# Performance work log

Measured on AMD Instinct MI355X. Metric: run time of the kernel, lower is better.

## Reference

```python
import jax, jax.numpy as jnp
import numpy as np
from jax import lax

DN = ('NCHW', 'OIHW', 'NCHW')
NUM_CODES = 8192


def _conv(x, w, b):
    # Conv2d(k=4, s=2, p=1)
    y = lax.conv_general_dilated(x, w, (2, 2), ((1, 1), (1, 1)), dimension_numbers=DN)
    return y + b[None, :, None, None]


def _convT(x, w, b):
    # ConvTranspose2d(k=4, s=2, p=1) as lhs-dilated conv; kernel already in equivalent OIHW layout
    y = lax.conv_general_dilated(x, w, (1, 1), ((2, 2), (2, 2)), lhs_dilation=(2, 2), dimension_numbers=DN)
    return y + b[None, :, None, None]


def _aff(x, s, b):
    # eval-mode BatchNorm folded to per-channel affine
    return x * s[None, :, None, None] + b[None, :, None, None]


def _forward(x, ew1, eb1, bn1s, bn1b, ew2, eb2, bn2s, bn2b, ew3, eb3, bn3s, bn3b, ew4, eb4, embed, cluster_size, dw1, db1, dbn1s, dbn1b, dw2, db2, dbn2s, dbn2b, dw3, db3, dbn3s, dbn3b, dw4, db4):
    sg = lax.stop_gradient
    embed = sg(embed)          # codebook is a torch buffer -> no grad
    cluster_size = sg(cluster_size)
    relu = jax.nn.relu
    # ---- Encoder: 4 stride-2 convs ----
    h = relu(_aff(_conv(x, ew1, eb1), bn1s, bn1b))
    h = relu(_aff(_conv(h, ew2, eb2), bn2s, bn2b))
    h = relu(_aff(_conv(h, ew3, eb3), bn3s, bn3b))
    z = _conv(h, ew4, eb4)                       # [B, D, G, G]
    zt = jnp.transpose(z, (0, 2, 3, 1))          # [B, G, G, D]
    D = zt.shape[-1]
    flat = zt.reshape(-1, D)                     # [N, D]
    N = flat.shape[0]
    # ---- VQ: pairwise squared distance + argmin codebook lookup ----
    dist = (flat * flat).sum(1, keepdims=True) - 2.0 * (flat @ embed.T) + (embed * embed).sum(1)[None, :]
    soft = jax.nn.softmax(-dist, axis=-1)        # temperature = 1.0
    codes = jnp.argmin(dist, axis=1)             # [N]
    zq = embed[codes]                            # [N, D]
    commitment_loss = jnp.mean((flat - sg(zq)) ** 2)
    codebook_loss = jnp.mean((zq - sg(flat)) ** 2)
    avg_soft = soft.mean(0)
    usage_entropy = -(avg_soft * jnp.log(avg_soft + 1e-10)).sum()
    diversity_loss = -usage_entropy / float(np.log(NUM_CODES))
    zq_st = flat + sg(zq - flat)                 # straight-through estimator
    zq_grid = jnp.transpose(zq_st.reshape(zt.shape), (0, 3, 1, 2))  # [B, D, G, G]
    # ---- Decoder: 4 stride-2 transposed convs ----
    h = relu(_aff(_convT(zq_grid, dw1, db1), dbn1s, dbn1b))
    h = relu(_aff(_convT(h, dw2, db2), dbn2s, dbn2b))
    h = relu(_aff(_convT(h, dw3, db3), dbn3s, dbn3b))
    recon = jax.nn.sigmoid(_convT(h, dw4, db4))
    recon_loss = jnp.mean((recon - x) ** 2)
    # ---- usage stats (no-grad in torch) ----
    hard_avg = jnp.zeros(NUM_CODES, flat.dtype).at[codes].add(1.0) / N
    perplexity = jnp.exp(-(hard_avg * jnp.log(hard_avg + 1e-10)).sum())
    active_codes = (cluster_size > 1).sum()
    codes_grid = codes.reshape(zt.shape[:-1])
    return (recon, recon_loss, codes_grid, zq_grid, commitment_loss, codebook_loss, diversity_loss, usage_entropy, perplexity, active_codes)


def setup_inputs() -> dict:
    keys = iter(jax.random.split(jax.random.key(0), 64))
    def randn(shape, s=1.0):
        return jax.random.normal(next(keys), shape, jnp.float32) * s
    def randu(shape):
        return jax.random.uniform(next(keys), shape, dtype=jnp.float32)
    B, H = 32, 256
    return {
        'x': randu((B, 1, H, H)),
        'ew1': randn((64, 1, 4, 4), 0.25), 'eb1': randn((64,), 0.1),
        'bn1s': randu((64,)), 'bn1b': randn((64,), 0.1),
        'ew2': randn((64, 64, 4, 4), 0.03), 'eb2': randn((64,), 0.1),
        'bn2s': randu((64,)), 'bn2b': randn((64,), 0.1),
        'ew3': randn((128, 64, 4, 4), 0.03), 'eb3': randn((128,), 0.1),
        'bn3s': randu((128,)), 'bn3b': randn((128,), 0.1),
        'ew4': randn((64, 128, 4, 4), 0.02), 'eb4': randn((64,), 0.1),
        'embed': randn((8192, 64), 0.5),
        'cluster_size': jnp.ones((8192,), jnp.float32),
        'dw1': randn((128, 64, 4, 4), 0.03), 'db1': randn((128,), 0.1),
        'dbn1s': randu((128,)), 'dbn1b': randn((128,), 0.1),
        'dw2': randn((64, 128, 4, 4), 0.02), 'db2': randn((64,), 0.1),
        'dbn2s': randu((64,)), 'dbn2b': randn((64,), 0.1),
        'dw3': randn((64, 64, 4, 4), 0.03), 'db3': randn((64,), 0.1),
        'dbn3s': randu((64,)), 'dbn3b': randn((64,), 0.1),
        'dw4': randn((1, 64, 4, 4), 0.03), 'db4': randn((1,), 0.1),
    }


def reference(x, ew1, eb1, bn1s, bn1b, ew2, eb2, bn2s, bn2b, ew3, eb3, bn3s, bn3b, ew4, eb4, embed, cluster_size, dw1, db1, dbn1s, dbn1b, dw2, db2, dbn2s, dbn2b, dw3, db3, dbn3s, dbn3b, dw4, db4):
    return _forward(x, ew1, eb1, bn1s, bn1b, ew2, eb2, bn2s, bn2b, ew3, eb3, bn3s, bn3b, ew4, eb4, embed, cluster_size, dw1, db1, dbn1s, dbn1b, dw2, db2, dbn2s, dbn2b, dw3, db3, dbn3s, dbn3b, dw4, db4)
```

## Files before the change

### kernel.cpp

```cpp
#include <hip/hip_runtime.h>
#include <cstdint>
#include <cstddef>


#define DEVI __device__ __forceinline__

typedef short  short8 __attribute__((ext_vector_type(8)));
typedef __bf16 bf16x8 __attribute__((ext_vector_type(8)));
typedef float  f32x16 __attribute__((ext_vector_type(16)));

DEVI f32x16 MFMA(bf16x8 a, bf16x8 b, f32x16 c){
  return __builtin_amdgcn_mfma_f32_32x32x16_bf16(a, b, c, 0, 0, 0);
}

DEVI ushort f2bf(float f){
  unsigned u = __float_as_uint(f);
  unsigned r = (u + 0x7FFFu + ((u >> 16) & 1u)) >> 16;
  return (ushort)r;
}
DEVI float bf2f(ushort h){ return __uint_as_float(((unsigned)h) << 16); }

union U8 { short8 s; bf16x8 b; };
DEVI bf16x8 ldg8u(const ushort* p){
  U8 u; u.s = *(const short8*)p; return u.b;
}

DEVI float wred64(float v){
  #pragma unroll
  for (int off=32; off>0; off>>=1) v += __shfl_down(v, off, 64);
  return v;
}

#define O_RECON     0
#define O_RLOSS     2097152
#define O_CODES     2097153
#define O_ZQ        2105345
#define O_COMMIT    2629633
#define O_CB        2629634
#define O_DIV       2629635
#define O_UE        2629636
#define O_PERP      2629637
#define O_ACT       2629638

#define WS_R1       0ull
#define A3H_OFF     0ull
#define A3M_OFF     8912896ull
#define A3L_OFF     17825792ull
#define PP_OFF      33554432ull
#define MT_OFF      37748736ull
#define PARTA_OFF   41943040ull
#define A2H_OFF     134217728ull
#define A2M_OFF     151519232ull
#define A2L_OFF     168820736ull
#define EH_OFF      134217728ull
#define EM_OFF      135266304ull
#define EL_OFF      136314880ull
#define FH_OFF      137363456ull
#define FM_OFF      138412032ull
#define FL_OFF      139460608ull
#define D2H_OFF     134217728ull
#define D2L_OFF     151519232ull
#define D1H_OFF     168820736ull
#define D1L_OFF     177733632ull
#define WS_FLAT     186646528ull
#define WS_ZQP      188743680ull
#define WS_WT       191102976ull
#define WT_E2       (WS_WT)
#define WT_E3       (WT_E2 + 393216ull)
#define WT_E4       (WT_E3 + 786432ull)
#define WT_D1       (WT_E4 + 786432ull)
#define WT_D2       (WT_D1 + 524288ull)
#define WT_D3       (WT_D2 + 524288ull)
#define WS_W4       (WT_D3 + 262144ull)
#define WS_STATS    (WS_W4 + 4096ull)
#define ST_RMP      (WS_STATS)
#define ST_CNT      (ST_RMP + 65536ull)
#define ST_AVGS     (ST_CNT + 32768ull)
#define ST_ROWZI    (ST_AVGS + 32768ull)
#define ST_CODESQ   (ST_ROWZI + 32768ull)
#define ST_LOSS     (ST_CODESQ + 32768ull)

__global__ __launch_bounds__(256) void k_init(unsigned int* __restrict__ cnt,
                                              unsigned long long* __restrict__ rmp,
                                              float* __restrict__ loss)
{
  int i = blockIdx.x*256 + threadIdx.x;
  if (i < 8192){ cnt[i]=0u; rmp[i]=0xFFFFFFFFFFFFFFFFull; }
  if (i < 8) loss[i]=0.f;
}

__global__ __launch_bounds__(256) void k_wsplit(
    const float* __restrict__ src, ushort* __restrict__ dh,
    ushort* __restrict__ dm, ushort* __restrict__ dl,
    int OC, int CIN, int isT, int three)
{
  int i = blockIdx.x*256 + threadIdx.x;
  if (i >= 16*OC*CIN) return;
  int cin = i % CIN; int t = i / CIN; int oc = t % OC; int tap = t / OC;
  int st;
  if (isT){
    int pq = tap>>2, ab = tap&3;
    int p = pq>>1, q = pq&1, a = ab>>1, b = ab&1;
    st = (p + 2*a)*4 + (q + 2*b);
  } else st = tap;
  float v = src[((size_t)oc*CIN + cin)*16 + st];
  ushort h = f2bf(v); float r = v - bf2f(h);
  if (three){
    ushort m = f2bf(r); float r2 = r - bf2f(m);
    dm[i] = m; dl[i] = f2bf(r2);
  } else {
    dl[i] = f2bf(r);
  }
  dh[i] = h;
}

__global__ __launch_bounds__(256) void k_w4prep(const float* __restrict__ dw4,
                                                float* __restrict__ w4)
{
  int i = blockIdx.x*256 + threadIdx.x;
  if (i >= 1024) return;
  int c = i & 63; int t16 = i >> 6;
  int pq = t16 >> 2, ab = t16 & 3;
  int p = pq>>1, q = pq&1, a = ab>>1, b = ab&1;
  w4[i] = dw4[(size_t)c*16 + (p+2*a)*4 + (q+2*b)];
}

__global__ __launch_bounds__(256) void k_esplit(
    const float* __restrict__ src, ushort* __restrict__ dh,
    ushort* __restrict__ dm, ushort* __restrict__ dl)
{
  int i = blockIdx.x*256 + threadIdx.x;
  float v = src[i];
  ushort h = f2bf(v); float r1 = v - bf2f(h);
  ushort m = f2bf(r1); float r2 = r1 - bf2f(m);
  dh[i] = h; dm[i] = m; dl[i] = f2bf(r2);
}

__global__ __launch_bounds__(256) void k_zpad3(unsigned* __restrict__ b0,
                                               unsigned* __restrict__ b1,
                                               unsigned* __restrict__ b2,
                                               int rows, int Wp, int cwords)
{
  int i = blockIdx.x*256 + threadIdx.x;
  int total = rows*2*cwords;
  if (i >= total) return;
  int pos = i / cwords, cw = i % cwords;
  int row = pos >> 1, side = pos & 1;
  size_t w = ((size_t)row*Wp + (side ? (Wp-1) : 0))*cwords + cw;
  b0[w] = 0u;
  if (b1) b1[w] = 0u;
  if (b2) b2[w] = 0u;
}

__global__ __launch_bounds__(256) void enc_conv1(
    const float* __restrict__ x, const float* __restrict__ w,
    const float* __restrict__ cb_, const float* __restrict__ bns,
    const float* __restrict__ bnb, float* __restrict__ out)
{
  __shared__ __align__(16) float sIn[34][36];
  __shared__ __align__(16) float sW[64][16];
  int b = blockIdx.x;
  int t = b & 63, n = b >> 6;
  int ty = t >> 3, tx = t & 7;
  int oy0 = ty*16, ox0 = tx*16;
  int iy0 = 2*oy0 - 1, ix0 = 2*ox0 - 1;
  int tid = threadIdx.x;
  int spg = tid & 31, og = tid >> 5;
  int sy = spg >> 1, x0 = (spg & 1)*8;

  if (tid < 64){
    const float* wp = w + tid*16;
    *(float4*)&sW[tid][0]  = *(const float4*)(wp);
    *(float4*)&sW[tid][4]  = *(const float4*)(wp+4);
    *(float4*)&sW[tid][8]  = *(const float4*)(wp+8);
    *(float4*)&sW[tid][12] = *(const float4*)(wp+12);
  }
  for (int e = tid; e < 34*34; e += 256){
    int rr = e/34, cc = e%34;
    int iy = iy0+rr, ix = ix0+cc;
    float v = 0.f;
    if ((unsigned)iy < 256u && (unsigned)ix < 256u)
      v = x[(size_t)n*65536 + iy*256 + ix];
    sIn[rr][cc] = v;
  }
  __syncthreads();

  float acc[8][8];
  #pragma unroll
  for (int j=0;j<8;j++)
    #pragma unroll
    for (int xi=0;xi<8;xi++) acc[j][xi]=0.f;

  #pragma unroll
  for (int ky=0; ky<4; ky++){
    int riy = 2*sy + ky;
    float seg[20];
    #pragma unroll
    for (int i=0;i<5;i++){
      float4 v = *(const float4*)&sIn[riy][2*x0 + 4*i];
      seg[4*i+0]=v.x; seg[4*i+1]=v.y; seg[4*i+2]=v.z; seg[4*i+3]=v.w;
    }
    #pragma unroll
    for (int j=0;j<8;j++){
      float4 w4v = *(const float4*)&sW[og*8+j][ky*4];
      #pragma unroll
      for (int xi=0; xi<8; xi++){
        acc[j][xi] = fmaf(seg[2*xi+0], w4v.x,
                     fmaf(seg[2*xi+1], w4v.y,
                     fmaf(seg[2*xi+2], w4v.z,
                     fmaf(seg[2*xi+3], w4v.w, acc[j][xi]))));
      }
    }
  }

  float sc[8], sh[8];
  #pragma unroll
  for (int j=0;j<8;j++){
    int oc = og*8+j;
    sc[j] = bns[oc];
    sh[j] = fmaf(cb_[oc], sc[j], bnb[oc]);
  }
  int oy = oy0 + sy;
  #pragma unroll
  for (int xi=0; xi<8; xi++){
    int oxg = ox0 + x0 + xi;
    float* op = out + (((size_t)n*128 + oy)*128 + oxg)*64 + og*8;
    float4 q0, q1;
    q0.x = fmaxf(fmaf(acc[0][xi], sc[0], sh[0]), 0.f);
    q0.y = fmaxf(fmaf(acc[1][xi], sc[1], sh[1]), 0.f);
    q0.z = fmaxf(fmaf(acc[2][xi], sc[2], sh[2]), 0.f);
    q0.w = fmaxf(fmaf(acc[3][xi], sc[3], sh[3]), 0.f);
    q1.x = fmaxf(fmaf(acc[4][xi], sc[4], sh[4]), 0.f);
    q1.y = fmaxf(fmaf(acc[5][xi], sc[5], sh[5]), 0.f);
    q1.z = fmaxf(fmaf(acc[6][xi], sc[6], sh[6]), 0.f);
    q1.w = fmaxf(fmaf(acc[7][xi], sc[7], sh[7]), 0.f);
    *(float4*)op     = q0;
    *(float4*)(op+4) = q1;
  }
}

template<int CIN, int OC, int OUTW, int OUTH, int INW, int INH, bool XPAD,
         int INMODE, int OUTMODE>
__global__ __launch_bounds__(256) void enc_conv(
    const float* __restrict__ in,
    const ushort* __restrict__ aH, const ushort* __restrict__ aM,
    const ushort* __restrict__ aL,
    const ushort* __restrict__ wtH, const ushort* __restrict__ wtM,
    const ushort* __restrict__ wtL,
    const float* __restrict__ cb_, const float* __restrict__ bns,
    const float* __restrict__ bnb,
    float* __restrict__ outF,
    ushort* __restrict__ oH, ushort* __restrict__ oM, ushort* __restrict__ oL,
    int nOcg)
{
  constexpr int INWP  = (INMODE==1) ? (INW+2) : (XPAD ? (INW+2) : INW);
  constexpr int WP    = INW + 2;
  constexpr int NROWS = 64 / OUTW;
  constexpr int AELEM = NROWS * WP * CIN;
  constexpr int BCIN  = (CIN > 64) ? 64 : CIN;
  constexpr int BELEM = 64 * BCIN;
  constexpr int SCRSZ = (3*BELEM*2 > 64*68*4) ? 3*BELEM*2 : 64*68*4;

  __shared__ __align__(16) ushort sAh[AELEM], sAm[AELEM], sAl[AELEM];
  __shared__ __align__(16) char sScr[SCRSZ];
  ushort* sBh = (ushort*)sScr;
  ushort* sBm = sBh + BELEM;
  ushort* sBl = sBm + BELEM;
  float*  sC  = (float*)sScr;

  int b = blockIdx.x;
  int ocg = b % nOcg; b /= nOcg;
  int yb  = b % (OUTH/NROWS); b /= (OUTH/NROWS);
  int n = b;
  int oy0 = yb * NROWS, oc0 = ocg * 64;

  int tid = threadIdx.x;
  int l = tid & 63, wave = tid >> 6;
  int wm = wave >> 1, wn = wave & 1;
  int r = l & 31, kp = l >> 5;
  int idx = wm*32 + r;
  int oy_off = idx / OUTW, ox = idx % OUTW;

  f32x16 acc;
  #pragma unroll
  for (int i=0;i<16;i++) acc[i] = 0.f;

  const size_t nbase = (size_t)n * INH * INWP * CIN;

  for (int ky = 0; ky < 4; ky++){
    __syncthreads();
    for (int c = tid; c < AELEM/8; c += 256){
      int j  = c / (WP*CIN/8);
      int rm = c % (WP*CIN/8);
      int lx = rm / (CIN/8);
      int c8 = (rm % (CIN/8)) * 8;
      int iy = 2*(oy0 + j) - 1 + ky;
      bool ok = (unsigned)iy < (unsigned)INH;
      unsigned off = (unsigned)(((j*WP + lx)*CIN + c8)*2) ^ ((((unsigned)lx>>1)&7u)<<4);
      if constexpr (INMODE == 0){
        int gx = XPAD ? lx : (lx - 1);
        if (!XPAD) ok = ok && ((unsigned)gx < (unsigned)INW);
        float4 v0 = {0,0,0,0}, v1 = {0,0,0,0};
        if (ok){
          const float* s = in + nbase + ((size_t)iy*INWP + gx)*CIN + c8;
          v0 = *(const float4*)s; v1 = *(const float4*)(s+4);
        }
        float vv[8] = {v0.x,v0.y,v0.z,v0.w,v1.x,v1.y,v1.z,v1.w};
        short8 hh, mm, ll;
        #pragma unroll
        for (int e=0;e<8;e++){
          ushort h = f2bf(vv[e]); float r1 = vv[e] - bf2f(h);
          ushort m = f2bf(r1);    float r2 = r1 - bf2f(m);
          hh[e] = (short)h; mm[e] = (short)m; ll[e] = (short)f2bf(r2);
        }
        *(short8*)((char*)sAh + off) = hh;
        *(short8*)((char*)sAm + off) = mm;
        *(short8*)((char*)sAl + off) = ll;
      } else {
        short8 vh = {0,0,0,0,0,0,0,0}, vm = vh, vl = vh;
        if (ok){
          size_t s = nbase + ((size_t)iy*INWP + lx)*CIN + c8;
          vh = *(const short8*)(aH + s);
          vm = *(const short8*)(aM + s);
          vl = *(const short8*)(aL + s);
        }
        *(short8*)((char*)sAh + off) = vh;
        *(short8*)((char*)sAm + off) = vm;
        *(short8*)((char*)sAl + off) = vl;
      }
    }
    for (int kx = 0; kx < 4; kx++){
      int tap = ky*4 + kx;
      for (int ch = 0; ch < CIN; ch += BCIN){
        __syncthreads();
        for (int c = tid; c < BELEM/8; c += 256){
          int oc = c / (BCIN/8);
          int c8 = (c % (BCIN/8)) * 8;
          size_t s = ((size_t)tap*OC + oc0 + oc)*CIN + ch + c8;
          unsigned off = (unsigned)((oc*BCIN + c8)*2) ^ (((unsigned)oc&7u)<<4);
          *(short8*)((char*)sBh + off) = *(const short8*)(wtH + s);
          *(short8*)((char*)sBm + off) = *(const short8*)(wtM + s);
          *(short8*)((char*)sBl + off) = *(const short8*)(wtL + s);
        }
        __syncthreads();
        int lx = 2*ox + kx;
        unsigned asw  = ((((unsigned)lx>>1)&7u)<<4);
        unsigned alin = (unsigned)(((oy_off*WP + lx)*CIN)*2);
        int ocl = wn*32 + r;
        unsigned bsw  = (((unsigned)ocl&7u)<<4);
        unsigned blin = (unsigned)((ocl*BCIN)*2);
        #pragma unroll
        for (int ct = 0; ct < BCIN/16; ct++){
          unsigned kbA = (unsigned)((ch + ct*16 + kp*8)*2);
          unsigned kbB = (unsigned)((ct*16 + kp*8)*2);
          unsigned ao = (alin + kbA) ^ asw;
          unsigned bo = (blin + kbB) ^ bsw;
          bf16x8 ah = *(const bf16x8*)((char*)sAh + ao);
          bf16x8 am = *(const bf16x8*)((char*)sAm + ao);
          bf16x8 al = *(const bf16x8*)((char*)sAl + ao);
          bf16x8 bh = *(const bf16x8*)((char*)sBh + bo);
          bf16x8 bm = *(const bf16x8*)((char*)sBm + bo);
          bf16x8 bl = *(const bf16x8*)((char*)sBl + bo);
          acc = MFMA(ah, bh, acc);
          acc = MFMA(ah, bm, acc);
          acc = MFMA(am, bh, acc);
          acc = MFMA(ah, bl, acc);
          acc = MFMA(am, bm, acc);
          acc = MFMA(al, bh, acc);
        }
      }
    }
  }
  __syncthreads();
  #pragma unroll
  for (int q = 0; q < 16; q++){
    int rowt = (q&3) + 8*(q>>2) + 4*kp;
    sC[(wm*32 + rowt)*68 + wn*32 + r] = acc[q];
  }
  __syncthreads();
  {
    int m = tid >> 2, qq = tid & 3;
    int oc = oc0 + qq*16;
    int oyg = oy0 + m / OUTW;
    int oxg = m % OUTW;
    if constexpr (OUTMODE == 1){
      size_t row = (size_t)n*256 + oyg*16 + oxg;
      float* op = outF + row*64 + qq*16;
      size_t pb = row*64 + qq*16;
      short8 hv[2], mv[2], lv[2];
      #pragma unroll
      for (int i=0;i<16;i++){
        float v = sC[m*68 + qq*16 + i] + cb_[oc+i];
        op[i] = v;
        ushort h = f2bf(v); float r1 = v - bf2f(h);
        ushort mm = f2bf(r1); float r2 = r1 - bf2f(mm);
        hv[i>>3][i&7]=(short)h; mv[i>>3][i&7]=(short)mm; lv[i>>3][i&7]=(short)f2bf(r2);
      }
      *(short8*)(oH + pb) = hv[0]; *(short8*)(oH + pb + 8) = hv[1];
      *(short8*)(oM + pb) = mv[0]; *(short8*)(oM + pb + 8) = mv[1];
      *(short8*)(oL + pb) = lv[0]; *(short8*)(oL + pb + 8) = lv[1];
    } else {
      size_t pbase = (((size_t)n*OUTH + oyg)*(OUTW+2) + oxg + 1)*OC + oc;
      short8 hv[2], mv[2], lv[2];
      #pragma unroll
      for (int i=0;i<16;i++){
        float s1 = bns[oc+i];
        float s2 = fmaf(cb_[oc+i], s1, bnb[oc+i]);
        float v = fmaxf(fmaf(sC[m*68 + qq*16 + i], s1, s2), 0.f);
        ushort h = f2bf(v); float r1 = v - bf2f(h);
        ushort mm = f2bf(r1); float r2 = r1 - bf2f(mm);
        hv[i>>3][i&7]=(short)h; mv[i>>3][i&7]=(short)mm; lv[i>>3][i&7]=(short)f2bf(r2);
      }
      *(short8*)(oH + pbase)   = hv[0]; *(short8*)(oH + pbase+8) = hv[1];
      *(short8*)(oM + pbase)   = mv[0]; *(short8*)(oM + pbase+8) = mv[1];
      *(short8*)(oL + pbase)   = lv[0]; *(short8*)(oL + pbase+8) = lv[1];
    }
  }
}

__global__ __launch_bounds__(256) void k_codesq(const float* __restrict__ embed,
                                                float* __restrict__ codesq)
{
  int j = blockIdx.x*4 + (threadIdx.x>>6);
  int c = threadIdx.x & 63;
  float e = embed[(size_t)j*64 + c];
  float s = wred64(e*e);
  if (c==0) codesq[j] = s;
}

DEVI float rmp_minval(unsigned long long v){
  unsigned skey = (unsigned)(v >> 32);
  unsigned u = (skey & 0x80000000u) ? (skey ^ 0x80000000u) : ~skey;
  return __uint_as_float(u);
}

__global__ __launch_bounds__(256) void vq_min(
    const ushort* __restrict__ fH, const ushort* __restrict__ fM,
    const ushort* __restrict__ fL,
    const ushort* __restrict__ eH, const ushort* __restrict__ eM,
    const ushort* __restrict__ eL,
    const float* __restrict__ codesq,
    unsigned long long* __restrict__ rmp,
    float* __restrict__ Pp, float* __restrict__ Mt)
{
  __shared__ __align__(16) ushort sAh[128*64], sAm[128*64], sAl[128*64];
  int cb = blockIdx.x & 63, rb = blockIdx.x >> 6;
  int row0 = rb*128, c0 = cb*128;
  int tid = threadIdx.x, l = tid&63, wave = tid>>6;
  int wm = wave>>1, wn = wave&1, r = l&31, kp = l>>5;

  for (int c = tid; c < 1024; c += 256){
    int rr = c >> 3, c8 = (c & 7)*8;
    size_t s = (size_t)(row0+rr)*64 + c8;
    unsigned off = (unsigned)((rr*64 + c8)*2) ^ (((unsigned)rr&7u)<<4);
    *(short8*)((char*)sAh + off) = *(const short8*)(fH + s);
    *(short8*)((char*)sAm + off) = *(const short8*)(fM + s);
    *(short8*)((char*)sAl + off) = *(const short8*)(fL + s);
  }
  __syncthreads();

  f32x16 acc[2][2];
  #pragma unroll
  for (int mt=0;mt<2;mt++)
    #pragma unroll
    for (int nt=0;nt<2;nt++)
      #pragma unroll
      for (int i=0;i<16;i++) acc[mt][nt][i]=0.f;

  #pragma unroll
  for (int ks=0; ks<4; ks++){
    unsigned kb = (unsigned)((ks*16 + kp*8)*2);
    int ko = ks*16 + kp*8;
    bf16x8 Ah[2],Am[2],Al[2],Bh[2],Bm[2],Bl[2];
    #pragma unroll
    for (int mt=0;mt<2;mt++){
      int rowi = wm*64 + mt*32 + r;
      unsigned o = ((unsigned)(rowi*128) + kb) ^ (((unsigned)rowi&7u)<<4);
      Ah[mt] = *(const bf16x8*)((char*)sAh + o);
      Am[mt] = *(const bf16x8*)((char*)sAm + o);
      Al[mt] = *(const bf16x8*)((char*)sAl + o);
    }
    #pragma unroll
    for (int nt=0;nt<2;nt++){
      int coli = c0 + wn*64 + nt*32 + r;
      size_t bo = (size_t)coli*64 + ko;
      Bh[nt] = ldg8u(eH + bo);
      Bm[nt] = ldg8u(eM + bo);
      Bl[nt] = ldg8u(eL + bo);
    }
    #pragma unroll
    for (int mt=0;mt<2;mt++)
      #pragma unroll
      for (int nt=0;nt<2;nt++){
        acc[mt][nt] = MFMA(Ah[mt], Bh[nt], acc[mt][nt]);
        acc[mt][nt] = MFMA(Ah[mt], Bm[nt], acc[mt][nt]);
        acc[mt][nt] = MFMA(Am[mt], Bh[nt], acc[mt][nt]);
        acc[mt][nt] = MFMA(Ah[mt], Bl[nt], acc[mt][nt]);
        acc[mt][nt] = MFMA(Am[mt], Bm[nt], acc[mt][nt]);
        acc[mt][nt] = MFMA(Al[mt], Bh[nt], acc[mt][nt]);
      }
  }

  float cq[2];
  cq[0] = codesq[c0 + wn*64 + r];
  cq[1] = codesq[c0 + wn*64 + 32 + r];
  #pragma unroll
  for (int mt=0; mt<2; mt++){
    #pragma unroll
    for (int q=0; q<16; q++){
      int rowt = (q&3) + 8*(q>>2) + 4*kp;
      int grow = row0 + wm*64 + mt*32 + rowt;
      float dv[2];
      unsigned long long kmin = 0xFFFFFFFFFFFFFFFFull;
      #pragma unroll
      for (int nt=0; nt<2; nt++){
        int col = c0 + wn*64 + nt*32 + r;
        float d = cq[nt] - 2.f*acc[mt][nt][q];
        dv[nt] = d;
        unsigned u = __float_as_uint(d);
        unsigned sgn = (unsigned)((int)u >> 31);
        unsigned skey = u ^ (sgn | 0x80000000u);
        unsigned long long key = (((unsigned long long)skey)<<32) | (unsigned)col;
        if (key < kmin) kmin = key;
      }
      #pragma unroll
      for (int off2=16; off2>0; off2>>=1){
        unsigned long long o2 = __shfl_xor(kmin, off2, 64);
        if (o2 < kmin) kmin = o2;
      }
      float mloc = rmp_minval(kmin);
      float p = __expf(mloc - dv[0]) + __expf(mloc - dv[1]);
      #pragma unroll
      for (int off2=16; off2>0; off2>>=1) p += __shfl_xor(p, off2, 64);
      if (r == 0){
        atomicMin(&rmp[grow], kmin);
        size_t pidx = (size_t)grow*128 + (size_t)cb*2 + wn;
        Pp[pidx] = p;
        Mt[pidx] = mloc;
      }
    }
  }
}

__global__ __launch_bounds__(256) void k_rowz2(
    const unsigned long long* __restrict__ rmp,
    const float* __restrict__ Pp, const float* __restrict__ Mt,
    float* __restrict__ rowzi)
{
  int row = blockIdx.x*256 + threadIdx.x;
  float mg = rmp_minval(rmp[row]);
  const float* pp = Pp + (size_t)row*128;
  const float* mt = Mt + (size_t)row*128;
  float z = 0.f;
  for (int t = 0; t < 128; t++)
    z = fmaf(__expf(mg - mt[t]), pp[t], z);
  rowzi[row] = 1.f / z;
}

__global__ __launch_bounds__(256) void vq_avg(
    const ushort* __restrict__ fH, const ushort* __restrict__ fM,
    const ushort* __restrict__ fL,
    const ushort* __restrict__ eH, const ushort* __restrict__ eM,
    const ushort* __restrict__ eL,
    const float* __restrict__ codesq,
    const unsigned long long* __restrict__ rmp,
    const float* __restrict__ rowzi,
    float* __restrict__ partA)
{
  __shared__ __align__(16) ushort sAh[128*64], sAm[128*64], sAl[128*64];
  __shared__ float colbuf[128];
  int cb = blockIdx.x & 63, rb = blockIdx.x >> 6;
  int row0 = rb*128, c0 = cb*128;
  int tid = threadIdx.x, l = tid&63, wave = tid>>6;
  int wm = wave>>1, wn = wave&1, r = l&31, kp = l>>5;

  if (tid < 128) colbuf[tid] = 0.f;

  for (int c = tid; c < 1024; c += 256){
    int rr = c >> 3, c8 = (c & 7)*8;
    size_t s = (size_t)(row0+rr)*64 + c8;
    unsigned off = (unsigned)((rr*64 + c8)*2) ^ (((unsigned)rr&7u)<<4);
    *(short8*)((char*)sAh + off) = *(const short8*)(fH + s);
    *(short8*)((char*)sAm + off) = *(const short8*)(fM + s);
    *(short8*)((char*)sAl + off) = *(const short8*)(fL + s);
  }
  __syncthreads();

  f32x16 acc[2][2];
  #pragma unroll
  for (int mt=0;mt<2;mt++)
    #pragma unroll
    for (int nt=0;nt<2;nt++)
      #pragma unroll
      for (int i=0;i<16;i++) acc[mt][nt][i]=0.f;

  #pragma unroll
  for (int ks=0; ks<4; ks++){
    unsigned kb = (unsigned)((ks*16 + kp*8)*2);
    int ko = ks*16 + kp*8;
    bf16x8 Ah[2],Am[2],Al[2],Bh[2],Bm[2],Bl[2];
    #pragma unroll
    for (int mt=0;mt<2;mt++){
      int rowi = wm*64 + mt*32 + r;
      unsigned o = ((unsigned)(rowi*128) + kb) ^ (((unsigned)rowi&7u)<<4);
      Ah[mt] = *(const bf16x8*)((char*)sAh + o);
      Am[mt] = *(const bf16x8*)((char*)sAm + o);
      Al[mt] = *(const bf16x8*)((char*)sAl + o);
    }
    #pragma unroll
    for (int nt=0;nt<2;nt++){
      int coli = c0 + wn*64 + nt*32 + r;
      size_t bo = (size_t)coli*64 + ko;
      Bh[nt] = ldg8u(eH + bo);
      Bm[nt] = ldg8u(eM + bo);
      Bl[nt] = ldg8u(eL + bo);
    }
    #pragma unroll
    for (int mt=0;mt<2;mt++)
      #pragma unroll
      for (int nt=0;nt<2;nt++){
        acc[mt][nt] = MFMA(Ah[mt], Bh[nt], acc[mt][nt]);
        acc[mt][nt] = MFMA(Ah[mt], Bm[nt], acc[mt][nt]);
        acc[mt][nt] = MFMA(Am[mt], Bh[nt], acc[mt][nt]);
        acc[mt][nt] = MFMA(Ah[mt], Bl[nt], acc[mt][nt]);
        acc[mt][nt] = MFMA(Am[mt], Bm[nt], acc[mt][nt]);
        acc[mt][nt] = MFMA(Al[mt], Bh[nt], acc[mt][nt]);
      }
  }

  float cq[2];
  cq[0] = codesq[c0 + wn*64 + r];
  cq[1] = codesq[c0 + wn*64 + 32 + r];
  float colacc[2] = {0.f, 0.f};
  #pragma unroll
  for (int mt=0; mt<2; mt++){
    #pragma unroll
    for (int q=0; q<16; q++){
      int rowt = (q&3) + 8*(q>>2) + 4*kp;
      int grow = row0 + wm*64 + mt*32 + rowt;
      float mi = rmp_minval(rmp[grow]);
      float zi = rowzi[grow];
      #pragma unroll
      for (int nt=0; nt<2; nt++){
        float d = cq[nt] - 2.f*acc[mt][nt][q];
        colacc[nt] = fmaf(__expf(mi - d), zi, colacc[nt]);
      }
    }
  }
  #pragma unroll
  for (int nt=0; nt<2; nt++){
    float o = __shfl_xor(colacc[nt], 32, 64);
    colacc[nt] += o;
    if (l < 32) atomicAdd(&colbuf[wn*64 + nt*32 + r], colacc[nt]);
  }
  __syncthreads();
  if (tid < 128)
    partA[(size_t)rb*8192 + c0 + tid] = colbuf[tid];
}

__global__ __launch_bounds__(256) void k_avgred(const float* __restrict__ partA,
                                                float* __restrict__ avgs)
{
  int j = blockIdx.x*256 + threadIdx.x;
  float s = 0.f;
  for (int rb = 0; rb < 64; rb++)
    s += partA[(size_t)rb*8192 + j];
  avgs[j] = s;
}

__global__ __launch_bounds__(256) void vq_post(
    const float* __restrict__ flat, const float* __restrict__ embed,
    const unsigned long long* __restrict__ rmp,
    float* __restrict__ out_codes, float* __restrict__ out_zq,
    ushort* __restrict__ zqPh, ushort* __restrict__ zqPl,
    float* __restrict__ loss, unsigned int* __restrict__ cnt)
{
  int r = blockIdx.x*4 + (threadIdx.x>>6);
  int c = threadIdx.x & 63;
  unsigned j = (unsigned)(rmp[r] & 0xFFFFFFFFull);
  float e = embed[(size_t)j*64 + c];
  float f = flat[(size_t)r*64 + c];
  int n = r>>8, rem = r&255, gy = rem>>4, gx = rem&15;
  out_zq[(((size_t)n*64 + c)*16 + gy)*16 + gx] = e;
  ushort h = f2bf(e);
  size_t pz = (((size_t)n*16 + gy)*18 + gx + 1)*64 + c;
  zqPh[pz] = h; zqPl[pz] = f2bf(e - bf2f(h));
  float d = f - e;
  float s2 = wred64(d*d);
  if (c==0){
    out_codes[r] = (float)j;
    atomicAdd(cnt + j, 1u);
    atomicAdd(loss + 1, s2);
  }
}

template<int CIN, int OC, int SW, int SH, bool OUTPAD, int OMODE>
__global__ __launch_bounds__(256) void dec_convT(
    const ushort* __restrict__ inH, const ushort* __restrict__ inL,
    const ushort* __restrict__ wtH, const ushort* __restrict__ wtL,
    const float* __restrict__ db, const float* __restrict__ bns,
    const float* __restrict__ bnb,
    ushort* __restrict__ oH, ushort* __restrict__ oL,
    float* __restrict__ outF, int nOcg)
{
  constexpr int TR    = 64 / SW;
  constexpr int NRA   = TR + 1;
  constexpr int WPin  = SW + 2;
  constexpr int AELEM = NRA * WPin * CIN;
  constexpr int OUTH  = 2*SH;
  constexpr int OW    = OUTPAD ? (2*SW+2) : (2*SW);
  constexpr int SMSZ  = (2*AELEM*2 > 64*68*4) ? 2*AELEM*2 : 64*68*4;

  __shared__ __align__(16) char smem[SMSZ];
  ushort* sAh = (ushort*)smem;
  ushort* sAl = sAh + AELEM;
  float*  sC  = (float*)smem;

  int b = blockIdx.x;
  int par = b & 3; b >>= 2;
  int ocg = b % nOcg; b /= nOcg;
  int tb = b % (SH/TR); b /= (SH/TR);
  int n = b;
  int p = par >> 1, q = par & 1;
  int t0 = tb * TR, oc0 = ocg * 64;

  int tid = threadIdx.x, l = tid&63, wave = tid>>6;
  int wm = wave>>1, wn = wave&1;
  int r = l&31, kp = l>>5;
  int idx = wm*32 + r;
  int t_off = idx / SW, s = idx % SW;
  int ocl = oc0 + wn*32 + r;

  f32x16 acc;
  #pragma unroll
  for (int i=0;i<16;i++) acc[i]=0.f;

  for (int c = tid; c < AELEM/8; c += 256){
    int j  = c / (WPin*CIN/8);
    int rm = c % (WPin*CIN/8);
    int lx = rm / (CIN/8);
    int c8 = (rm % (CIN/8)) * 8;
    int giy = t0 + p - 1 + j;
    bool ok = (unsigned)giy < (unsigned)SH;
    short8 vh = {0,0,0,0,0,0,0,0}, vl = {0,0,0,0,0,0,0,0};
    if (ok){
      size_t sidx = (((size_t)n*SH + giy)*WPin + lx)*CIN + c8;
      vh = *(const short8*)(inH + sidx);
      vl = *(const short8*)(inL + sidx);
    }
    unsigned off = (unsigned)(((j*WPin + lx)*CIN + c8)*2) ^ (((unsigned)lx&7u)<<4);
    *(short8*)((char*)sAh + off) = vh;
    *(short8*)((char*)sAl + off) = vl;
  }
  __syncthreads();

  for (int ab = 0; ab < 4; ab++){
    int a = ab>>1, bb = ab&1;
    int lx = s + q + bb;
    int rs = t_off + a;
    unsigned asw  = (((unsigned)lx&7u)<<4);
    unsigned alin = (unsigned)(((rs*WPin + lx)*CIN)*2);
    size_t brow = ((size_t)(par*4 + ab)*OC + ocl)*CIN;
    #pragma unroll
    for (int ct = 0; ct < CIN/16; ct++){
      int ko = ct*16 + kp*8;
      unsigned ao = (alin + (unsigned)(ko*2)) ^ asw;
      bf16x8 ah = *(const bf16x8*)((char*)sAh + ao);
      bf16x8 al = *(const bf16x8*)((char*)sAl + ao);
      bf16x8 bh = ldg8u(wtH + brow + ko);
      bf16x8 bl = ldg8u(wtL + brow + ko);
      acc = MFMA(ah, bh, acc);
      acc = MFMA(ah, bl, acc);
      acc = MFMA(al, bh, acc);
    }
  }
  __syncthreads();
  #pragma unroll
  for (int qre = 0; qre < 16; qre++){
    int rowt = (qre&3) + 8*(qre>>2) + 4*kp;
    sC[(wm*32 + rowt)*68 + wn*32 + r] = acc[qre];
  }
  __syncthreads();
  {
    int m = tid >> 2, qq = tid & 3;
    int oc = oc0 + qq*16;
    int y  = 2*(t0 + m/SW) + p;
    int xs = m % SW;
    int xp = OUTPAD ? (2*xs + q + 1) : (2*xs + q);
    size_t base = (((size_t)n*OUTH + y)*OW + xp)*OC + oc;
    if constexpr (OMODE == 1){
      #pragma unroll
      for (int i=0;i<16;i+=4){
        float4 o4; float tmp[4];
        #pragma unroll
        for (int u=0; u<4; u++){
          float s1 = bns[oc+i+u];
          float s2 = fmaf(db[oc+i+u], s1, bnb[oc+i+u]);
          tmp[u] = fmaxf(fmaf(sC[m*68 + qq*16 + i+u], s1, s2), 0.f);
        }
        o4.x=tmp[0]; o4.y=tmp[1]; o4.z=tmp[2]; o4.w=tmp[3];
        *(float4*)(outF + base + i) = o4;
      }
    } else {
      short8 h0[2], l0[2];
      #pragma unroll
      for (int i=0;i<16;i++){
        float s1 = bns[oc+i];
        float s2 = fmaf(db[oc+i], s1, bnb[oc+i]);
        float v = fmaxf(fmaf(sC[m*68 + qq*16 + i], s1, s2), 0.f);
        ushort h = f2bf(v);
        ushort lo = f2bf(v - bf2f(h));
        h0[i>>3][i&7]=(short)h; l0[i>>3][i&7]=(short)lo;
      }
      *(short8*)(oH + base)     = h0[0];
      *(short8*)(oH + base + 8) = h0[1];
      *(short8*)(oL + base)     = l0[0];
      *(short8*)(oL + base + 8) = l0[1];
    }
  }
}

__global__ __launch_bounds__(256) void dec_convT4(
    const float* __restrict__ d3, const float* __restrict__ w4,
    const float* __restrict__ db4, const float* __restrict__ xref,
    float* __restrict__ recon, float* __restrict__ loss)
{
  __shared__ __align__(16) float sT[10*10*68];
  __shared__ __align__(16) float sWt[16*64];
  __shared__ float red[4];
  int b = blockIdx.x;
  int t = b & 255, n = b >> 8;
  int ty = t >> 4, tx = t & 15;
  int y0 = ty*16, x0 = tx*16;
  int r0 = y0/2 - 1, c0 = x0/2 - 1;
  int tid = threadIdx.x;

  *(float4*)&sWt[tid*4] = *(const float4*)(w4 + tid*4);

  const float* base = d3 + (size_t)n*128*128*64;
  for (int e = tid; e < 1600; e += 256){
    int rr = e/160; int rem = e%160; int cc = rem/16; int c4 = (rem%16)*4;
    int gr = r0+rr, gc = c0+cc;
    float4 v = {0,0,0,0};
    if ((unsigned)gr<128u && (unsigned)gc<128u)
      v = *(const float4*)(base + ((size_t)gr*128+gc)*64 + c4);
    *(float4*)&sT[(rr*10+cc)*68 + c4] = v;
  }
  __syncthreads();

  int sy = tid>>4, sx = tid&15;
  int p = sy&1, q = sx&1;
  int lr0 = (sy>>1)+p, lc0 = (sx>>1)+q;
  int par = p*2+q;
  float4 a4 = {0,0,0,0};
  #pragma unroll
  for (int a=0;a<2;a++){
    #pragma unroll
    for (int bb=0;bb<2;bb++){
      const float* ip = &sT[((lr0+a)*10 + lc0+bb)*68];
      const float* wp = &sWt[(par*4+a*2+bb)*64];
      #pragma unroll
      for (int c=0;c<64;c+=4){
        float4 v  = *(const float4*)(ip+c);
        float4 wv = *(const float4*)(wp+c);
        a4.x = fmaf(v.x, wv.x, a4.x);
        a4.y = fmaf(v.y, wv.y, a4.y);
        a4.z = fmaf(v.z, wv.z, a4.z);
        a4.w = fmaf(v.w, wv.w, a4.w);
      }
    }
  }
  float acc = (a4.x + a4.y) + (a4.z + a4.w);
  float v = acc + db4[0];
  float rcn = 1.f/(1.f + __expf(-v));
  int y = y0+sy, x = x0+sx;
  size_t oi = (size_t)n*65536 + (size_t)y*256 + x;
  recon[oi] = rcn;
  float d = rcn - xref[oi];
  float s2 = wred64(d*d);
  if ((tid & 63)==0) red[tid>>6] = s2;
  __syncthreads();
  if (tid==0) atomicAdd(loss + 0, red[0]+red[1]+red[2]+red[3]);
}

__global__ __launch_bounds__(256) void k_final(
    const float* __restrict__ avgs, const unsigned int* __restrict__ cnt,
    const float* __restrict__ cluster, const float* __restrict__ loss,
    float* __restrict__ dout)
{
  __shared__ float red[3][4];
  int tid = threadIdx.x;
  float e1=0.f, e2=0.f, ac=0.f;
  for (int j=tid; j<8192; j+=256){
    float a = avgs[j] * (1.f/8192.f);
    e1 += a * __logf(a + 1e-10f);
    float h = (float)cnt[j] * (1.f/8192.f);
    e2 += h * __logf(h + 1e-10f);
    ac += (cluster[j] > 1.f) ? 1.f : 0.f;
  }
  e1 = wred64(e1); e2 = wred64(e2); ac = wred64(ac);
  int wv = tid >> 6;
  if ((tid & 63)==0){ red[0][wv]=e1; red[1][wv]=e2; red[2][wv]=ac; }
  __syncthreads();
  if (tid==0){
    float s1 = red[0][0]+red[0][1]+red[0][2]+red[0][3];
    float s2 = red[1][0]+red[1][1]+red[1][2]+red[1][3];
    float s3 = red[2][0]+red[2][1]+red[2][2]+red[2][3];
    float ue = -s1;
    dout[O_RLOSS]  = loss[0] * (1.f/2097152.f);
    float cc = loss[1] * (1.f/524288.f);
    dout[O_COMMIT] = cc;
    dout[O_CB]     = cc;
    dout[O_DIV]    = -ue / 9.010913347279288f;
    dout[O_UE]     = ue;
    dout[O_PERP]   = __expf(-s2);
    dout[O_ACT]    = s3;
  }
}

extern "C" void kernel_launch(void* const* d_in, const int* in_sizes, int n_in,
                              void* d_out, int out_size, void* d_ws, size_t ws_size,
                              hipStream_t stream)
{
  (void)in_sizes; (void)n_in; (void)out_size; (void)ws_size;
  const float* x     = (const float*)d_in[0];
  const float* ew1   = (const float*)d_in[1];
  const float* eb1   = (const float*)d_in[2];
  const float* bn1s  = (const float*)d_in[3];
  const float* bn1b  = (const float*)d_in[4];
  const float* ew2   = (const float*)d_in[5];
  const float* eb2   = (const float*)d_in[6];
  const float* bn2s  = (const float*)d_in[7];
  const float* bn2b  = (const float*)d_in[8];
  const float* ew3   = (const float*)d_in[9];
  const float* eb3   = (const float*)d_in[10];
  const float* bn3s  = (const float*)d_in[11];
  const float* bn3b  = (const float*)d_in[12];
  const float* ew4   = (const float*)d_in[13];
  const float* eb4   = (const float*)d_in[14];
  const float* embed = (const float*)d_in[15];
  const float* clsz  = (const float*)d_in[16];
  const float* dw1   = (const float*)d_in[17];
  const float* db1   = (const float*)d_in[18];
  const float* dbn1s = (const float*)d_in[19];
  const float* dbn1b = (const float*)d_in[20];
  const float* dw2   = (const float*)d_in[21];
  const float* db2   = (const float*)d_in[22];
  const float* dbn2s = (const float*)d_in[23];
  const float* dbn2b = (const float*)d_in[24];
  const float* dw3   = (const float*)d_in[25];
  const float* db3   = (const float*)d_in[26];
  const float* dbn3s = (const float*)d_in[27];
  const float* dbn3b = (const float*)d_in[28];
  const float* dw4   = (const float*)d_in[29];
  const float* db4   = (const float*)d_in[30];

  float* out = (float*)d_out;
  uint8_t* wsb = (uint8_t*)d_ws;

  float*  A1   = (float*)(wsb + WS_R1);
  float*  D3f  = (float*)(wsb + WS_R1);
  ushort* A3h  = (ushort*)(wsb + A3H_OFF);
  ushort* A3m  = (ushort*)(wsb + A3M_OFF);
  ushort* A3l  = (ushort*)(wsb + A3L_OFF);
  float*  Pp   = (float*)(wsb + PP_OFF);
  float*  Mt   = (float*)(wsb + MT_OFF);
  float*  partA= (float*)(wsb + PARTA_OFF);
  ushort* A2h  = (ushort*)(wsb + A2H_OFF);
  ushort* A2m  = (ushort*)(wsb + A2M_OFF);
  ushort* A2l  = (ushort*)(wsb + A2L_OFF);
  ushort* eH   = (ushort*)(wsb + EH_OFF);
  ushort* eM   = (ushort*)(wsb + EM_OFF);
  ushort* eL   = (ushort*)(wsb + EL_OFF);
  ushort* fH   = (ushort*)(wsb + FH_OFF);
  ushort* fM   = (ushort*)(wsb + FM_OFF);
  ushort* fL   = (ushort*)(wsb + FL_OFF);
  ushort* D1h  = (ushort*)(wsb + D1H_OFF);
  ushort* D1l  = (ushort*)(wsb + D1L_OFF);
  ushort* D2h  = (ushort*)(wsb + D2H_OFF);
  ushort* D2l  = (ushort*)(wsb + D2L_OFF);
  float*  flat = (float*)(wsb + WS_FLAT);
  ushort* zqPh = (ushort*)(wsb + WS_ZQP);
  ushort* zqPl = (ushort*)(wsb + WS_ZQP + 1179648ull);

  ushort* wE2h = (ushort*)(wsb + WT_E2);
  ushort* wE2m = wE2h + 65536;  ushort* wE2l = wE2m + 65536;
  ushort* wE3h = (ushort*)(wsb + WT_E3);
  ushort* wE3m = wE3h + 131072; ushort* wE3l = wE3m + 131072;
  ushort* wE4h = (ushort*)(wsb + WT_E4);
  ushort* wE4m = wE4h + 131072; ushort* wE4l = wE4m + 131072;
  ushort* wD1h = (ushort*)(wsb + WT_D1);
  ushort* wD1l = wD1h + 131072;
  ushort* wD2h = (ushort*)(wsb + WT_D2);
  ushort* wD2l = wD2h + 131072;
  ushort* wD3h = (ushort*)(wsb + WT_D3);
  ushort* wD3l = wD3h + 65536;
  float*  w4   = (float*)(wsb + WS_W4);

  unsigned long long* rmp = (unsigned long long*)(wsb + ST_RMP);
  unsigned int* cnt = (unsigned int*)(wsb + ST_CNT);
  float* avgs   = (float*)(wsb + ST_AVGS);
  float* rowzi  = (float*)(wsb + ST_ROWZI);
  float* codesq = (float*)(wsb + ST_CODESQ);
  float* loss   = (float*)(wsb + ST_LOSS);

  dim3 B(256);

  k_init<<<32, B, 0, stream>>>(cnt, rmp, loss);

  k_wsplit<<<256, B, 0, stream>>>(ew2, wE2h, wE2m, wE2l, 64, 64, 0, 1);
  k_wsplit<<<512, B, 0, stream>>>(ew3, wE3h, wE3m, wE3l, 128, 64, 0, 1);
  k_wsplit<<<512, B, 0, stream>>>(ew4, wE4h, wE4m, wE4l, 64, 128, 0, 1);
  k_wsplit<<<512, B, 0, stream>>>(dw1, wD1h, nullptr, wD1l, 128, 64, 1, 0);
  k_wsplit<<<512, B, 0, stream>>>(dw2, wD2h, nullptr, wD2l, 64, 128, 1, 0);
  k_wsplit<<<256, B, 0, stream>>>(dw3, wD3h, nullptr, wD3l, 64, 64, 1, 0);
  k_w4prep<<<4, B, 0, stream>>>(dw4, w4);

  k_zpad3<<<512, B, 0, stream>>>((unsigned*)A2h, (unsigned*)A2m, (unsigned*)A2l,
                                 32*64, 66, 32);
  k_zpad3<<<128, B, 0, stream>>>((unsigned*)zqPh, (unsigned*)zqPl, nullptr,
                                 32*16, 18, 32);

  enc_conv1<<<2048, B, 0, stream>>>(x, ew1, eb1, bn1s, bn1b, A1);
  enc_conv<64,64,64,64,128,128,false,0,0><<<2048, B, 0, stream>>>(
      A1, nullptr, nullptr, nullptr, wE2h, wE2m, wE2l, eb2, bn2s, bn2b,
      nullptr, A2h, A2m, A2l, 1);
  k_zpad3<<<512, B, 0, stream>>>((unsigned*)A3h, (unsigned*)A3m, (unsigned*)A3l,
                                 32*32, 34, 64);
  enc_conv<64,128,32,32,64,64,true,1,0><<<1024, B, 0, stream>>>(
      nullptr, A2h, A2m, A2l, wE3h, wE3m, wE3l, eb3, bn3s, bn3b,
      nullptr, A3h, A3m, A3l, 2);
  k_esplit<<<2048, B, 0, stream>>>(embed, eH, eM, eL);
  enc_conv<128,64,16,16,32,32,true,1,1><<<128, B, 0, stream>>>(
      nullptr, A3h, A3m, A3l, wE4h, wE4m, wE4l, eb4, eb4, eb4,
      flat, fH, fM, fL, 1);

  k_codesq<<<2048, B, 0, stream>>>(embed, codesq);

  vq_min<<<4096, B, 0, stream>>>(fH, fM, fL, eH, eM, eL, codesq, rmp, Pp, Mt);
  k_rowz2<<<32, B, 0, stream>>>(rmp, Pp, Mt, rowzi);
  vq_avg<<<4096, B, 0, stream>>>(fH, fM, fL, eH, eM, eL, codesq, rmp, rowzi, partA);
  k_avgred<<<32, B, 0, stream>>>(partA, avgs);

  vq_post<<<2048, B, 0, stream>>>(flat, embed, rmp, out + O_CODES, out + O_ZQ,
                                  zqPh, zqPl, loss, cnt);

  k_zpad3<<<512, B, 0, stream>>>((unsigned*)D1h, (unsigned*)D1l, nullptr, 32*32, 34, 64);
  k_zpad3<<<512, B, 0, stream>>>((unsigned*)D2h, (unsigned*)D2l, nullptr, 32*64, 66, 32);

  dec_convT<64,128,16,16,true,0><<<1024, B, 0, stream>>>(
      zqPh, zqPl, wD1h, wD1l, db1, dbn1s, dbn1b, D1h, D1l, nullptr, 2);
  dec_convT<128,64,32,32,true,0><<<2048, B, 0, stream>>>(
      D1h, D1l, wD2h, wD2l, db2, dbn2s, dbn2b, D2h, D2l, nullptr, 1);
  dec_convT<64,64,64,64,false,1><<<8192, B, 0, stream>>>(
      D2h, D2l, wD3h, wD3l, db3, dbn3s, dbn3b, nullptr, nullptr, D3f, 1);
  dec_convT4<<<8192, B, 0, stream>>>(D3f, w4, db4, x, out + O_RECON, loss);

  k_final<<<1, B, 0, stream>>>(avgs, cnt, clsz, loss, out);
}
```

Before: 1.110 ms.

## Process multiple convT output parities per block and store dec3 output as bf16

Decoder transposed-conv kernels now loop over 2 or 4 output parity classes inside one block. The loaded input tile is shared across them, so each tile is read once instead of four times and fewer blocks are launched. The third decoder layer writes its activations as a single bf16 plane instead of fp32, and the final convT kernel reads bf16 and widens to float, halving that tensor's traffic. In exchange each block does more serial work, uses separate shared buffers that raise LDS usage and may lower occupancy, and the bf16 intermediate loses precision versus the previous fp32 path.

```diff
diff --git a/kernel.cpp b/kernel.cpp
--- a/kernel.cpp
+++ b/kernel.cpp
@@ -694,35 +694,32 @@
   }
 }
 
-template<int CIN, int OC, int SW, int SH, bool OUTPAD, int OMODE>
-__global__ __launch_bounds__(256) void dec_convT(
+template<int CIN, int OC, int SW, int SH, bool OUTPAD, int OMODE, int NPAR>
+__global__ __launch_bounds__(256) void dec_convT_m(
     const ushort* __restrict__ inH, const ushort* __restrict__ inL,
     const ushort* __restrict__ wtH, const ushort* __restrict__ wtL,
     const float* __restrict__ db, const float* __restrict__ bns,
     const float* __restrict__ bnb,
-    ushort* __restrict__ oH, ushort* __restrict__ oL,
-    float* __restrict__ outF, int nOcg)
+    ushort* __restrict__ oH, ushort* __restrict__ oL, int nOcg)
 {
   constexpr int TR    = 64 / SW;
-  constexpr int NRA   = TR + 1;
+  constexpr int NRA   = TR + ((NPAR==4) ? 2 : 1);
   constexpr int WPin  = SW + 2;
   constexpr int AELEM = NRA * WPin * CIN;
   constexpr int OUTH  = 2*SH;
   constexpr int OW    = OUTPAD ? (2*SW+2) : (2*SW);
-  constexpr int SMSZ  = (2*AELEM*2 > 64*68*4) ? 2*AELEM*2 : 64*68*4;
-
-  __shared__ __align__(16) char smem[SMSZ];
-  ushort* sAh = (ushort*)smem;
-  ushort* sAl = sAh + AELEM;
-  float*  sC  = (float*)smem;
+
+  __shared__ __align__(16) ushort sAh[AELEM], sAl[AELEM];
+  __shared__ __align__(16) float sC[64*68];
 
   int b = blockIdx.x;
-  int par = b & 3; b >>= 2;
+  int p_blk = 0;
+  if (NPAR == 2){ p_blk = b & 1; b >>= 1; }
   int ocg = b % nOcg; b /= nOcg;
   int tb = b % (SH/TR); b /= (SH/TR);
   int n = b;
-  int p = par >> 1, q = par & 1;
   int t0 = tb * TR, oc0 = ocg * 64;
+  const int ROWBASE = (NPAR==4) ? -1 : (p_blk - 1);
 
   int tid = threadIdx.x, l = tid&63, wave = tid>>6;
   int wm = wave>>1, wn = wave&1;
@@ -731,16 +728,12 @@
   int t_off = idx / SW, s = idx % SW;
   int ocl = oc0 + wn*32 + r;
 
-  f32x16 acc;
-  #pragma unroll
-  for (int i=0;i<16;i++) acc[i]=0.f;
-
   for (int c = tid; c < AELEM/8; c += 256){
     int j  = c / (WPin*CIN/8);
     int rm = c % (WPin*CIN/8);
     int lx = rm / (CIN/8);
     int c8 = (rm % (CIN/8)) * 8;
-    int giy = t0 + p - 1 + j;
+    int giy = t0 + ROWBASE + j;
     bool ok = (unsigned)giy < (unsigned)SH;
     short8 vh = {0,0,0,0,0,0,0,0}, vl = {0,0,0,0,0,0,0,0};
     if (ok){
@@ -754,74 +747,83 @@
   }
   __syncthreads();
 
-  for (int ab = 0; ab < 4; ab++){
-    int a = ab>>1, bb = ab&1;
-    int lx = s + q + bb;
-    int rs = t_off + a;
-    unsigned asw  = (((unsigned)lx&7u)<<4);
-    unsigned alin = (unsigned)(((rs*WPin + lx)*CIN)*2);
-    size_t brow = ((size_t)(par*4 + ab)*OC + ocl)*CIN;
-    #pragma unroll
-    for (int ct = 0; ct < CIN/16; ct++){
-      int ko = ct*16 + kp*8;
-      unsigned ao = (alin + (unsigned)(ko*2)) ^ asw;
-      bf16x8 ah = *(const bf16x8*)((char*)sAh + ao);
-      bf16x8 al = *(const bf16x8*)((char*)sAl + ao);
-      bf16x8 bh = ldg8u(wtH + brow + ko);
-      bf16x8 bl = ldg8u(wtL + brow + ko);
-      acc = MFMA(ah, bh, acc);
-      acc = MFMA(ah, bl, acc);
-      acc = MFMA(al, bh, acc);
-    }
-  }
-  __syncthreads();
-  #pragma unroll
-  for (int qre = 0; qre < 16; qre++){
-    int rowt = (qre&3) + 8*(qre>>2) + 4*kp;
-    sC[(wm*32 + rowt)*68 + wn*32 + r] = acc[qre];
-  }
-  __syncthreads();
-  {
-    int m = tid >> 2, qq = tid & 3;
-    int oc = oc0 + qq*16;
-    int y  = 2*(t0 + m/SW) + p;
-    int xs = m % SW;
-    int xp = OUTPAD ? (2*xs + q + 1) : (2*xs + q);
-    size_t base = (((size_t)n*OUTH + y)*OW + xp)*OC + oc;
-    if constexpr (OMODE == 1){
-      #pragma unroll
-      for (int i=0;i<16;i+=4){
-        float4 o4; float tmp[4];
+  for (int pr = 0; pr < NPAR; pr++){
+    int p2 = (NPAR==4) ? (pr>>1) : p_blk;
+    int q2 = (NPAR==4) ? (pr&1)  : pr;
+    int par = p2*2 + q2;
+
+    f32x16 acc;
+    #pragma unroll
+    for (int i=0;i<16;i++) acc[i]=0.f;
+
+    for (int ab = 0; ab < 4; ab++){
+      int a = ab>>1, bb = ab&1;
+      int rs = t_off + ((NPAR==4) ? (p2 + a) : a);
+      int lx = s + q2 + bb;
+      unsigned asw  = (((unsigned)lx&7u)<<4);
+      unsigned alin = (unsigned)(((rs*WPin + lx)*CIN)*2);
+      size_t brow = ((size_t)(par*4 + ab)*OC + ocl)*CIN;
+      #pragma unroll
+      for (int ct = 0; ct < CIN/16; ct++){
+        int ko = ct*16 + kp*8;
+        unsigned ao = (alin + (unsigned)(ko*2)) ^ asw;
+        bf16x8 ah = *(const bf16x8*)((char*)sAh + ao);
+        bf16x8 al = *(const bf16x8*)((char*)sAl + ao);
+        bf16x8 bh = ldg8u(wtH + brow + ko);
+        bf16x8 bl = ldg8u(wtL + brow + ko);
+        acc = MFMA(ah, bh, acc);
+        acc = MFMA(ah, bl, acc);
+        acc = MFMA(al, bh, acc);
+      }
+    }
+
+    __syncthreads();
+    #pragma unroll
+    for (int qre = 0; qre < 16; qre++){
+      int rowt = (qre&3) + 8*(qre>>2) + 4*kp;
+      sC[(wm*32 + rowt)*68 + wn*32 + r] = acc[qre];
+    }
+    __syncthreads();
+    {
+      int m = tid >> 2, qq = tid & 3;
+      int oc = oc0 + qq*16;
+      int y  = 2*(t0 + m/SW) + p2;
+      int xs = m % SW;
+      int xp = OUTPAD ? (2*xs + q2 + 1) : (2*xs + q2);
+      size_t base = (((size_t)n*OUTH + y)*OW + xp)*OC + oc;
+      if constexpr (OMODE == 2){
+        short8 h0[2];
         #pragma unroll
-        for (int u=0; u<4; u++){
-          float s1 = bns[oc+i+u];
-          float s2 = fmaf(db[oc+i+u], s1, bnb[oc+i+u]);
-          tmp[u] = fmaxf(fmaf(sC[m*68 + qq*16 + i+u], s1, s2), 0.f);
+        for (int i=0;i<16;i++){
+          float s1 = bns[oc+i];
+          float s2 = fmaf(db[oc+i], s1, bnb[oc+i]);
+          float v = fmaxf(fmaf(sC[m*68 + qq*16 + i], s1, s2), 0.f);
+          h0[i>>3][i&7] = (short)f2bf(v);
         }
-        o4.x=tmp[0]; o4.y=tmp[1]; o4.z=tmp[2]; o4.w=tmp[3];
-        *(float4*)(outF + base + i) = o4;
-      }
-    } else {
-      short8 h0[2], l0[2];
-      #pragma unroll
-      for (int i=0;i<16;i++){
-        float s1 = bns[oc+i];
-        float s2 = fmaf(db[oc+i], s1, bnb[oc+i]);
-        float v = fmaxf(fmaf(sC[m*68 + qq*16 + i], s1, s2), 0.f);
-        ushort h = f2bf(v);
-        ushort lo = f2bf(v - bf2f(h));
-        h0[i>>3][i&7]=(short)h; l0[i>>3][i&7]=(short)lo;
-      }
-      *(short8*)(oH + base)     = h0[0];
-      *(short8*)(oH + base + 8) = h0[1];
-      *(short8*)(oL + base)     = l0[0];
-      *(short8*)(oL + base + 8) = l0[1];
+        *(short8*)(oH + base)     = h0[0];
+        *(short8*)(oH + base + 8) = h0[1];
+      } else {
+        short8 h0[2], l0[2];
+        #pragma unroll
+        for (int i=0;i<16;i++){
+          float s1 = bns[oc+i];
+          float s2 = fmaf(db[oc+i], s1, bnb[oc+i]);
+          float v = fmaxf(fmaf(sC[m*68 + qq*16 + i], s1, s2), 0.f);
+          ushort h = f2bf(v);
+          ushort lo = f2bf(v - bf2f(h));
+          h0[i>>3][i&7]=(short)h; l0[i>>3][i&7]=(short)lo;
+        }
+        *(short8*)(oH + base)     = h0[0];
+        *(short8*)(oH + base + 8) = h0[1];
+        *(short8*)(oL + base)     = l0[0];
+        *(short8*)(oL + base + 8) = l0[1];
+      }
     }
   }
 }
 
 __global__ __launch_bounds__(256) void dec_convT4(
-    const float* __restrict__ d3, const float* __restrict__ w4,
+    const ushort* __restrict__ d3, const float* __restrict__ w4,
     const float* __restrict__ db4, const float* __restrict__ xref,
     float* __restrict__ recon, float* __restrict__ loss)
 {
@@ -837,14 +839,21 @@
 
   *(float4*)&sWt[tid*4] = *(const float4*)(w4 + tid*4);
 
-  const float* base = d3 + (size_t)n*128*128*64;
-  for (int e = tid; e < 1600; e += 256){
-    int rr = e/160; int rem = e%160; int cc = rem/16; int c4 = (rem%16)*4;
+  const ushort* base = d3 + (size_t)n*128*128*64;
+  for (int e = tid; e < 800; e += 256){
+    int rr = e/80; int rem = e%80; int cc = rem/8; int c8 = (rem%8)*8;
     int gr = r0+rr, gc = c0+cc;
-    float4 v = {0,0,0,0};
+    short8 v = {0,0,0,0,0,0,0,0};
     if ((unsigned)gr<128u && (unsigned)gc<128u)
-      v = *(const float4*)(base + ((size_t)gr*128+gc)*64 + c4);
-    *(float4*)&sT[(rr*10+cc)*68 + c4] = v;
+      v = *(const short8*)(base + ((size_t)gr*128+gc)*64 + c8);
+    float* dst = &sT[(rr*10+cc)*68 + c8];
+    float4 f0, f1;
+    f0.x = bf2f((ushort)v[0]); f0.y = bf2f((ushort)v[1]);
+    f0.z = bf2f((ushort)v[2]); f0.w = bf2f((ushort)v[3]);
+    f1.x = bf2f((ushort)v[4]); f1.y = bf2f((ushort)v[5]);
+    f1.z = bf2f((ushort)v[6]); f1.w = bf2f((ushort)v[7]);
+    *(float4*)dst     = f0;
+    *(float4*)(dst+4) = f1;
   }
   __syncthreads();
 
@@ -959,7 +968,7 @@
   uint8_t* wsb = (uint8_t*)d_ws;
 
   float*  A1   = (float*)(wsb + WS_R1);
-  float*  D3f  = (float*)(wsb + WS_R1);
+  ushort* D3b  = (ushort*)(wsb + WS_R1);
   ushort* A3h  = (ushort*)(wsb + A3H_OFF);
   ushort* A3m  = (ushort*)(wsb + A3M_OFF);
   ushort* A3l  = (ushort*)(wsb + A3L_OFF);
@@ -1048,13 +1057,13 @@
   k_zpad3<<<512, B, 0, stream>>>((unsigned*)D1h, (unsigned*)D1l, nullptr, 32*32, 34, 64);
   k_zpad3<<<512, B, 0, stream>>>((unsigned*)D2h, (unsigned*)D2l, nullptr, 32*64, 66, 32);
 
-  dec_convT<64,128,16,16,true,0><<<1024, B, 0, stream>>>(
-      zqPh, zqPl, wD1h, wD1l, db1, dbn1s, dbn1b, D1h, D1l, nullptr, 2);
-  dec_convT<128,64,32,32,true,0><<<2048, B, 0, stream>>>(
-      D1h, D1l, wD2h, wD2l, db2, dbn2s, dbn2b, D2h, D2l, nullptr, 1);
-  dec_convT<64,64,64,64,false,1><<<8192, B, 0, stream>>>(
-      D2h, D2l, wD3h, wD3l, db3, dbn3s, dbn3b, nullptr, nullptr, D3f, 1);
-  dec_convT4<<<8192, B, 0, stream>>>(D3f, w4, db4, x, out + O_RECON, loss);
+  dec_convT_m<64,128,16,16,true,0,4><<<256, B, 0, stream>>>(
+      zqPh, zqPl, wD1h, wD1l, db1, dbn1s, dbn1b, D1h, D1l, 2);
+  dec_convT_m<128,64,32,32,true,0,2><<<1024, B, 0, stream>>>(
+      D1h, D1l, wD2h, wD2l, db2, dbn2s, dbn2b, D2h, D2l, 1);
+  dec_convT_m<64,64,64,64,false,2,4><<<2048, B, 0, stream>>>(
+      D2h, D2l, wD3h, wD3l, db3, dbn3s, dbn3b, D3b, nullptr, 1);
+  dec_convT4<<<8192, B, 0, stream>>>(D3b, w4, db4, x, out + O_RECON, loss);
 
   k_final<<<1, B, 0, stream>>>(avgs, cnt, clsz, loss, out);
 }
```

Result: faster. 1.088 ms (-2.0%).
